# Optimization experiments

Hardware: AMD Instinct MI355X
Metric: run time of the kernel (lower is better)

Reference implementation:

```python
import jax, jax.numpy as jnp
import numpy as np

VOCAB = 32000
EMBED = 512
HIDDEN = 1024
BATCH = 16
SEQ = 256


def setup_inputs() -> dict:
    key = jax.random.key(0)
    ks = jax.random.split(key, 12)
    E, H, V = EMBED, HIDDEN, VOCAB
    s_gate = 1.0 / np.sqrt(E + H)
    s_out = 1.0 / np.sqrt(H)
    return {
        "input": jax.random.randint(ks[0], (BATCH, SEQ), 0, V, dtype=jnp.int32),
        "embed": jax.random.normal(ks[1], (V, E), dtype=jnp.float32),
        "W_f": jax.random.normal(ks[2], (E + H, H), dtype=jnp.float32) * s_gate,
        "b_f": jax.random.normal(ks[3], (H,), dtype=jnp.float32) * s_gate,
        "W_i": jax.random.normal(ks[4], (E + H, H), dtype=jnp.float32) * s_gate,
        "b_i": jax.random.normal(ks[5], (H,), dtype=jnp.float32) * s_gate,
        "W_c": jax.random.normal(ks[6], (E + H, H), dtype=jnp.float32) * s_gate,
        "b_c": jax.random.normal(ks[7], (H,), dtype=jnp.float32) * s_gate,
        "W_o": jax.random.normal(ks[8], (E + H, H), dtype=jnp.float32) * s_gate,
        "b_o": jax.random.normal(ks[9], (H,), dtype=jnp.float32) * s_gate,
        "W_out": jax.random.normal(ks[10], (H, V), dtype=jnp.float32) * s_out,
        "b_out": jax.random.normal(ks[11], (V,), dtype=jnp.float32) * s_out,
    }


def reference(input, embed, W_f, b_f, W_i, b_i, W_c, b_c, W_o, b_o, W_out, b_out):
    B = input.shape[0]
    H = W_f.shape[1]
    tokens = embed[input]                     # [B, S, E]
    xs = jnp.swapaxes(tokens, 0, 1)           # [S, B, E] for scan over time

    def step(carry, x_t):
        h, c = carry
        catted = jnp.concatenate([x_t, h], axis=1)   # [B, E+H]
        f = jax.nn.sigmoid(catted @ W_f + b_f)
        i = jax.nn.sigmoid(catted @ W_i + b_i)
        cand = jnp.tanh(catted @ W_c + b_c)
        o = jax.nn.sigmoid(catted @ W_o + b_o)
        c = c * f + cand * i
        h = c * o
        return (h, c), h

    h0 = jnp.zeros((B, H), dtype=tokens.dtype)
    c0 = jnp.zeros((B, H), dtype=tokens.dtype)
    _, hs = jax.lax.scan(step, (h0, c0), xs)  # hs: [S, B, H]
    hiddens = jnp.swapaxes(hs, 0, 1)          # [B, S, H]
    return hiddens @ W_out + b_out            # [B, S, V]
```

## Files before the change

kernel.cpp:

```cpp
#include <hip/hip_runtime.h>
#include <hip/hip_bf16.h>

#define VOCAB  32000
#define EMBED  512
#define HIDDEN 1024
#define BATCH  16
#define SEQ    256
#define NROW   (BATCH*SEQ)
#define GCOLS  (4*HIDDEN)
#define NWREC  64
#define NWPACK 192
#define NTILE  8000
#define SENT32 0xFFFFFFFFu

typedef unsigned short u16;
typedef unsigned int   u32;
typedef unsigned long long u64;
typedef __attribute__((ext_vector_type(4))) float f32x4;
typedef __attribute__((ext_vector_type(8))) short bf16x8;
typedef __attribute__((ext_vector_type(8))) unsigned short u16x8;
typedef __attribute__((ext_vector_type(2))) unsigned long long u64x2;

__device__ inline u16 f2bf(float f){
  __hip_bfloat16 h = __float2bfloat16(f);
  return __builtin_bit_cast(u16, h);
}
__device__ inline void gload_lds16(const void* g, void* l){
  __builtin_amdgcn_global_load_lds((const __attribute__((address_space(1))) u32*)g,
                                   (__attribute__((address_space(3))) u32*)l, 16, 0, 0);
}
__device__ __forceinline__ u32 al32(const u32* p){
  return __hip_atomic_load(p, __ATOMIC_RELAXED, __HIP_MEMORY_SCOPE_AGENT);
}
__device__ __forceinline__ u64 al64(const u64* p){
  return __hip_atomic_load(p, __ATOMIC_RELAXED, __HIP_MEMORY_SCOPE_AGENT);
}
__device__ __forceinline__ void as32(u32* p, u32 v){
  __hip_atomic_store(p, v, __ATOMIC_RELAXED, __HIP_MEMORY_SCOPE_AGENT);
}
__device__ __forceinline__ void as64(u64* p, u64 v){
  __hip_atomic_store(p, v, __ATOMIC_RELAXED, __HIP_MEMORY_SCOPE_AGENT);
}

__global__ __launch_bounds__(256) void pack_gates(
    const float* __restrict__ Wf, const float* __restrict__ Wi,
    const float* __restrict__ Wc, const float* __restrict__ Wo,
    const float* __restrict__ bf_, const float* __restrict__ bi_,
    const float* __restrict__ bc_, const float* __restrict__ bo_,
    u16* __restrict__ Wxp, u16* __restrict__ Whp, float* __restrict__ bcat)
{
  const int NT_WX = (GCOLS/16)*(EMBED/32)*64;
  const int NT_WH = (GCOLS/16)*(HIDDEN/32)*64;
  int t = blockIdx.x*256 + threadIdx.x;
  if (t < NT_WX){
    int u = t;
    int lane = u&63; int kb = (u>>6)&15; int nblk = u>>10;
    int col = nblk*16 + (lane&15);
    int k0  = kb*32 + ((lane>>4)<<3);
    int g = col>>10, j = col&1023;
    const float* W = (g==0)?Wf:(g==1)?Wi:(g==2)?Wc:Wo;
    u16x8 v;
    #pragma unroll
    for (int e=0;e<8;e++) v[e] = f2bf(W[(size_t)(k0+e)*HIDDEN + j]);
    *(u16x8*)(Wxp + (size_t)u*8) = v;
  } else if (t < NT_WX + NT_WH){
    int u = t - NT_WX;
    int lane = u&63; int kb = (u>>6)&31; int nblk = u>>11;
    int col = nblk*16 + (lane&15);
    int k0  = kb*32 + ((lane>>4)<<3);
    int g = col>>10, j = col&1023;
    const float* W = (g==0)?Wf:(g==1)?Wi:(g==2)?Wc:Wo;
    u16x8 v;
    #pragma unroll
    for (int e=0;e<8;e++) v[e] = f2bf(W[(size_t)(EMBED + k0+e)*HIDDEN + j]);
    *(u16x8*)(Whp + (size_t)u*8) = v;
  } else {
    int u = t - NT_WX - NT_WH;
    if (u < GCOLS){
      int g = u>>10, j = u&1023;
      const float* B = (g==0)?bf_:(g==1)?bi_:(g==2)?bc_:bo_;
      bcat[u] = B[j];
    }
  }
}

__global__ __launch_bounds__(256) void gather_kernel(
    const int* __restrict__ tok, const float* __restrict__ embed, u16* __restrict__ Xg)
{
  int t = blockIdx.x*256 + threadIdx.x;
  int lane = t&63; int kb = (t>>6)&15; int mblk = t>>10;
  int s = mblk; int b = lane&15;
  int token = tok[b*SEQ + s];
  int k0 = kb*32 + ((lane>>4)<<3);
  const float* src = embed + (size_t)token*EMBED + k0;
  u16x8 v;
  #pragma unroll
  for (int e=0;e<8;e++) v[e] = f2bf(src[e]);
  *(u16x8*)(Xg + (size_t)t*8) = v;
}

template<int KB, bool REMAP>
__global__ __launch_bounds__(256,2) void gemm_pk(
    const u16* __restrict__ Ap, const u16* __restrict__ Bp,
    const float* __restrict__ bias, float* __restrict__ C,
    int Nblk128, int N)
{
  __shared__ u16 sm[8192];
  int tid = threadIdx.x; int lane = tid&63; int wv = tid>>6;
  int nwg = gridDim.x;
  int bid = blockIdx.x;
  int swz = (bid&7)*(nwg>>3) + (bid>>3);
  int bm = swz / Nblk128, bn = swz % Nblk128;
  int wr = wv>>1, wc = wv&1;
  f32x4 acc[4][4] = {};
  const u16* Abase = Ap + (size_t)(bm*8)*KB*512;
  const u16* Bbase = Bp + (size_t)(bn*8)*KB*512;
  for (int kb=0; kb<KB; ++kb){
    __syncthreads();
    #pragma unroll
    for (int c2=0;c2<4;c2++){
      int chunk = wv*4 + c2;
      const u16* g;
      if (chunk < 8) g = Abase + ((size_t)chunk*KB + kb)*512 + lane*8;
      else           g = Bbase + ((size_t)(chunk-8)*KB + kb)*512 + lane*8;
      gload_lds16(g, sm + chunk*512);
    }
    __syncthreads();
    bf16x8 a[4], b[4];
    #pragma unroll
    for (int m=0;m<4;m++) a[m] = *(const bf16x8*)(sm + (wr*4+m)*512 + lane*8);
    #pragma unroll
    for (int n=0;n<4;n++) b[n] = *(const bf16x8*)(sm + 4096 + (wc*4+n)*512 + lane*8);
    #pragma unroll
    for (int m=0;m<4;m++)
      #pragma unroll
      for (int n=0;n<4;n++)
        acc[m][n] = __builtin_amdgcn_mfma_f32_16x16x32_bf16(a[m], b[n], acc[m][n], 0,0,0);
  }
  int colb = bn*128 + wc*64;
  int rowb = bm*128 + wr*64;
  #pragma unroll
  for (int m=0;m<4;m++){
    int row0 = rowb + m*16 + (lane>>4)*4;
    #pragma unroll
    for (int n=0;n<4;n++){
      int col = colb + n*16 + (lane&15);
      float bv = bias[col];
      #pragma unroll
      for (int r2=0;r2<4;r2++){
        int row = row0 + r2;
        int orow = REMAP ? ((row&15)*SEQ + (row>>4)) : row;
        C[(size_t)orow*N + col] = acc[m][n][r2] + bv;
      }
    }
  }
}

__global__ __launch_bounds__(256,1) void lstm_fused(
    const u16* __restrict__ Whp, const float* __restrict__ Xpre,
    u16* hb, u16* Hp, u32* cnt, u32* tix, u32* packdone,
    const float* __restrict__ Wout, u16* __restrict__ Woutp,
    const float* __restrict__ bout, float* __restrict__ out)
{
  __shared__ char SMEM[148480];
  __shared__ u32 s_tick;
  u16* smWf = (u16*)SMEM;
  float (*gl)[16][17] = (float (*)[16][17])(SMEM + 131072);
  u16* smg = (u16*)SMEM;

  int tid = threadIdx.x; int lane = tid&63; int v = tid>>6;
  int w = blockIdx.x;

  if (w >= NWREC){
    const int NPK = (VOCAB/16)*(HIDDEN/32)*64;
    int u0 = (w - NWREC)*256 + tid;
    for (int u = u0; u < NPK; u += NWPACK*256){
      int l = u&63; int kb = (u>>6)&31; int nblk = u>>11;
      int col = nblk*16 + (l&15);
      int k0  = kb*32 + ((l>>4)<<3);
      u16x8 vv;
      #pragma unroll
      for (int e=0;e<8;e++) vv[e] = f2bf(Wout[(size_t)(k0+e)*VOCAB + col]);
      u64x2 t2 = __builtin_bit_cast(u64x2, vv);
      u64* dst = (u64*)(Woutp + (size_t)u*8);
      as64(dst+0, t2[0]);
      as64(dst+1, t2[1]);
    }
    asm volatile("s_waitcnt vmcnt(0)" ::: "memory");
    __syncthreads();
    if (tid==0) (void)__hip_atomic_fetch_add(packdone, 1u,
                       __ATOMIC_RELAXED, __HIP_MEMORY_SCOPE_AGENT);
  } else {
    #pragma unroll
    for (int f=0; f<32; ++f){
      int frag = v*32 + f;
      int g = frag>>5, kc = frag&31;
      const u16* src = Whp + ((size_t)(g*64 + w)*32 + kc)*512 + lane*8;
      gload_lds16(src, smWf + (size_t)frag*512);
    }
    asm volatile("s_waitcnt vmcnt(0)" ::: "memory");
    __syncthreads();

    float c = 0.f;
    int pb = tid>>4, pj = tid&15;
    int j = w*16 + pj;
    const int a_row = lane&15, a_k = (lane>>4)*8;
    const float* xb0 = Xpre + (size_t)pb*GCOLS + j;
    float x0 = xb0[0], x1 = xb0[1024], x2 = xb0[2048], x3 = xb0[3072];

    for (int s=0;s<SEQ;s++){
      const u16* rbuf = hb + (size_t)s*16384;
      u64 vv[16];
      for(;;){
        #pragma unroll
        for (int i=0;i<16;i++){
          const u64* p = (const u64*)(rbuf + a_row*1024 + (v*8+(i>>1))*32 + a_k) + (i&1);
          vv[i] = al64(p);
        }
        bool ok = true;
        #pragma unroll
        for (int i=0;i<16;i++)
          ok &= ((u32)vv[i]!=SENT32) & ((u32)(vv[i]>>32)!=SENT32);
        if (ok) break;
        __builtin_amdgcn_s_sleep(1);
      }
      bf16x8 af[8];
      #pragma unroll
      for (int i=0;i<8;i++){
        u64x2 t2 = {vv[2*i], vv[2*i+1]};
        af[i] = __builtin_bit_cast(bf16x8, t2);
      }
      f32x4 acc[4] = {};
      #pragma unroll
      for (int i=0;i<8;i++){
        #pragma unroll
        for (int g=0;g<4;g++){
          bf16x8 wfv = *(const bf16x8*)(smWf + ((size_t)(g*32 + v*8 + i))*512 + lane*8);
          acc[g] = __builtin_amdgcn_mfma_f32_16x16x32_bf16(af[i], wfv, acc[g], 0,0,0);
        }
      }
      {
        int jj = lane&15, b0 = (lane>>4)*4;
        #pragma unroll
        for (int g=0;g<4;g++)
          #pragma unroll
          for (int r2=0;r2<4;r2++)
            gl[v*4+g][b0+r2][jj] = acc[g][r2];
      }
      asm volatile("s_waitcnt lgkmcnt(0)" ::: "memory");
      __builtin_amdgcn_s_barrier();
      __builtin_amdgcn_sched_barrier(0);
      float xn0=0.f,xn1=0.f,xn2=0.f,xn3=0.f;
      if (s < SEQ-1){
        const float* xn = Xpre + ((size_t)(s+1)*16 + pb)*GCOLS + j;
        xn0 = xn[0]; xn1 = xn[1024]; xn2 = xn[2048]; xn3 = xn[3072];
      }
      float p0 = x0 + gl[0][pb][pj] + gl[4][pb][pj] + gl[ 8][pb][pj] + gl[12][pb][pj];
      float p1 = x1 + gl[1][pb][pj] + gl[5][pb][pj] + gl[ 9][pb][pj] + gl[13][pb][pj];
      float p2 = x2 + gl[2][pb][pj] + gl[6][pb][pj] + gl[10][pb][pj] + gl[14][pb][pj];
      float p3 = x3 + gl[3][pb][pj] + gl[7][pb][pj] + gl[11][pb][pj] + gl[15][pb][pj];
      float fg = 1.f/(1.f+__expf(-p0));
      float ig = 1.f/(1.f+__expf(-p1));
      float e2 = __expf(2.f*fminf(fmaxf(p2,-15.f),15.f));
      float cand = (e2-1.f)/(e2+1.f);
      float og = 1.f/(1.f+__expf(-p3));
      c = c*fg + cand*ig;
      float h = c*og;
      x0 = xn0; x1 = xn1; x2 = xn2; x3 = xn3;
      u32 hw_ = (u32)f2bf(h);
      u32 ow_ = (u32)__shfl_xor((int)hw_, 1);
      if ((pj&1)==0){
        u32 word = hw_ | (ow_<<16);
        if (s < SEQ-1){
          u16* wstep = hb + (size_t)(s+1)*16384;
          as32((u32*)wstep + (size_t)pb*512 + w*8 + (pj>>1), word);
        }
        as32((u32*)Hp + (size_t)s*8192 + (size_t)(j>>5)*256
                      + (size_t)(((j>>3)&3)*16 + pb)*4 + ((j&7)>>1), word);
      }
      __builtin_amdgcn_s_barrier();
      __builtin_amdgcn_sched_barrier(0);
      if ((s&7)==7){
        asm volatile("s_waitcnt vmcnt(0)" ::: "memory");
        __builtin_amdgcn_s_barrier();
        asm volatile("" ::: "memory");
        if (tid==0)
          (void)__hip_atomic_fetch_add(cnt + (size_t)(s>>3)*16, 1u,
                   __ATOMIC_RELAXED, __HIP_MEMORY_SCOPE_AGENT);
      }
    }
  }

  if (tid==0){
    while (al32(packdone) < (u32)NWPACK) __builtin_amdgcn_s_sleep(2);
  }
  __syncthreads();

  int wv = tid>>6;
  int wr = wv>>1, wc = wv&1;
  for(;;){
    __syncthreads();
    if (tid==0) s_tick = __hip_atomic_fetch_add(tix, 1u,
                   __ATOMIC_RELAXED, __HIP_MEMORY_SCOPE_AGENT);
    __syncthreads();
    u32 t = s_tick;
    if (t >= (u32)NTILE) break;
    int bm = (int)(t/250u), bn = (int)(t%250u);
    if (tid==0){
      while (al32(cnt + (size_t)bm*16) < (u32)NWREC)
        __builtin_amdgcn_s_sleep(2);
    }
    __syncthreads();
    const u16* Ab = Hp + (size_t)(bm*8)*32*512;
    const u16* Bb = Woutp + (size_t)(bn*8)*32*512;
    auto stage = [&](int kb, int bi){
      #pragma unroll
      for (int c2=0;c2<4;c2++){
        int chunk = wv*4 + c2;
        const u16* g;
        if (chunk < 8) g = Ab + ((size_t)chunk*32 + kb)*512 + lane*8;
        else           g = Bb + ((size_t)(chunk-8)*32 + kb)*512 + lane*8;
        gload_lds16(g, smg + (size_t)bi*8192 + chunk*512);
      }
    };
    stage(0,0); stage(1,1);
    f32x4 acc[4][4] = {};
    for (int kb=0; kb<32; ++kb){
      if (kb<31) asm volatile("s_waitcnt vmcnt(4)" ::: "memory");
      else       asm volatile("s_waitcnt vmcnt(0)" ::: "memory");
      __builtin_amdgcn_s_barrier();
      if (kb+2<32) stage(kb+2, (kb+2)%3);
      const u16* bufp = smg + (size_t)(kb%3)*8192;
      bf16x8 a[4], b[4];
      #pragma unroll
      for (int m=0;m<4;m++) a[m] = *(const bf16x8*)(bufp + (wr*4+m)*512 + lane*8);
      #pragma unroll
      for (int n=0;n<4;n++) b[n] = *(const bf16x8*)(bufp + 4096 + (wc*4+n)*512 + lane*8);
      #pragma unroll
      for (int m=0;m<4;m++)
        #pragma unroll
        for (int n=0;n<4;n++)
          acc[m][n] = __builtin_amdgcn_mfma_f32_16x16x32_bf16(a[m], b[n], acc[m][n], 0,0,0);
    }
    int colb = bn*128 + wc*64;
    int rowb = bm*128 + wr*64;
    #pragma unroll
    for (int m=0;m<4;m++){
      int row0 = rowb + m*16 + (lane>>4)*4;
      #pragma unroll
      for (int n=0;n<4;n++){
        int col = colb + n*16 + (lane&15);
        float bv = bout[col];
        #pragma unroll
        for (int r2=0;r2<4;r2++){
          int row = row0 + r2;
          int orow = (row&15)*SEQ + (row>>4);
          __builtin_nontemporal_store(acc[m][n][r2] + bv,
                                      &out[(size_t)orow*VOCAB + col]);
        }
      }
    }
  }
}

extern "C" void kernel_launch(void* const* d_in, const int* in_sizes, int n_in,
                              void* d_out, int out_size, void* d_ws, size_t ws_size,
                              hipStream_t stream)
{
  (void)in_sizes; (void)n_in; (void)out_size; (void)ws_size;
  const int*   tok   = (const int*)d_in[0];
  const float* embed = (const float*)d_in[1];
  const float* Wf    = (const float*)d_in[2];
  const float* bf_   = (const float*)d_in[3];
  const float* Wi    = (const float*)d_in[4];
  const float* bi_   = (const float*)d_in[5];
  const float* Wc    = (const float*)d_in[6];
  const float* bc_   = (const float*)d_in[7];
  const float* Wo    = (const float*)d_in[8];
  const float* bo_   = (const float*)d_in[9];
  const float* Wout  = (const float*)d_in[10];
  const float* bout  = (const float*)d_in[11];
  float* out = (float*)d_out;

  char* ws = (char*)d_ws;
  size_t off = 0;
  auto alloc = [&](size_t bytes)->void*{
    void* p = ws + off; off += (bytes + 255) & ~(size_t)255; return p;
  };
  u16*  Wxp   = (u16*)alloc((size_t)2097152*2);
  u16*  Xg    = (u16*)alloc((size_t)2097152*2);
  float* bcat = (float*)alloc((size_t)4096*4);
  u16*  hb    = (u16*)ws;
  u16*  Whp   = (u16*)alloc((size_t)4194304*2);
  u16*  Woutp = (u16*)alloc((size_t)32768000*2);
  float* Xpre = (float*)alloc((size_t)NROW*GCOLS*4);
  u16*  Hp    = (u16*)alloc((size_t)4194304*2);
  u32*  cnt   = (u32*)alloc((size_t)4096);
  u32*  tix   = (u32*)alloc((size_t)256);
  u32*  packdone = (u32*)alloc((size_t)256);

  pack_gates<<<3088, 256, 0, stream>>>(Wf,Wi,Wc,Wo, bf_,bi_,bc_,bo_,
                                       Wxp, Whp, bcat);
  gather_kernel<<<1024, 256, 0, stream>>>(tok, embed, Xg);
  gemm_pk<16,false><<<1024, 256, 0, stream>>>(Xg, Wxp, bcat, Xpre, 32, GCOLS);
  (void)hipMemsetAsync(hb, 0x00, 32768, stream);
  (void)hipMemsetAsync((char*)hb + 32768, 0xFF, 255*32768, stream);
  (void)hipMemsetAsync(cnt, 0, 4096 + 256 + 256, stream);
  lstm_fused<<<NWREC+NWPACK, 256, 0, stream>>>(Whp, Xpre, hb, Hp, cnt, tix,
                                               packdone, Wout, Woutp, bout, out);
}
```

Before: 1.169 ms.

## Replace per-step hidden buffer with double-buffered per-workgroup mailboxes

Instead of one shared hidden-state buffer per timestep that all 64 recurrent workgroups poll, each workgroup now gets its own double-buffered mailbox copy. Each writer broadcasts its h words into all 32 consumer copies, and readers reset their slot to the sentinel after consuming it. The aim is to cut contention on shared cache lines during the spin-wait and shrink the memset footprint. The next-step Xpre loads are also hoisted earlier, poll sleep intervals are raised, and output tiles are reordered so four row-blocks share a column tile. In exchange this adds many more global stores per step and a vmcnt wait before the broadcast.

```diff
diff --git a/kernel.cpp b/kernel.cpp
--- a/kernel.cpp
+++ b/kernel.cpp
@@ -158,7 +158,7 @@
 
 __global__ __launch_bounds__(256,1) void lstm_fused(
     const u16* __restrict__ Whp, const float* __restrict__ Xpre,
-    u16* hb, u16* Hp, u32* cnt, u32* tix, u32* packdone,
+    u16* mbox, u16* Hp, u32* cnt, u32* tix, u32* packdone,
     const float* __restrict__ Wout, u16* __restrict__ Woutp,
     const float* __restrict__ bout, float* __restrict__ out)
 {
@@ -209,12 +209,12 @@
     float x0 = xb0[0], x1 = xb0[1024], x2 = xb0[2048], x3 = xb0[3072];
 
     for (int s=0;s<SEQ;s++){
-      const u16* rbuf = hb + (size_t)s*16384;
+      const u16* rb = mbox + (size_t)((s+1)&1)*1048576 + (size_t)w*16384;
       u64 vv[16];
       for(;;){
         #pragma unroll
         for (int i=0;i<16;i++){
-          const u64* p = (const u64*)(rbuf + a_row*1024 + (v*8+(i>>1))*32 + a_k) + (i&1);
+          const u64* p = (const u64*)(rb + a_row*1024 + (v*8+(i>>1))*32 + a_k) + (i&1);
           vv[i] = al64(p);
         }
         bool ok = true;
@@ -224,6 +224,18 @@
         if (ok) break;
         __builtin_amdgcn_s_sleep(1);
       }
+      if (s < SEQ-1){
+        #pragma unroll
+        for (int i=0;i<16;i++){
+          u64* p = (u64*)(rb + a_row*1024 + (v*8+(i>>1))*32 + a_k) + (i&1);
+          as64(p, ~0ull);
+        }
+      }
+      float xn0=0.f,xn1=0.f,xn2=0.f,xn3=0.f;
+      if (s < SEQ-1){
+        const float* xn = Xpre + ((size_t)(s+1)*16 + pb)*GCOLS + j;
+        xn0 = xn[0]; xn1 = xn[1024]; xn2 = xn[2048]; xn3 = xn[3072];
+      }
       bf16x8 af[8];
       #pragma unroll
       for (int i=0;i<8;i++){
@@ -250,11 +262,6 @@
       asm volatile("s_waitcnt lgkmcnt(0)" ::: "memory");
       __builtin_amdgcn_s_barrier();
       __builtin_amdgcn_sched_barrier(0);
-      float xn0=0.f,xn1=0.f,xn2=0.f,xn3=0.f;
-      if (s < SEQ-1){
-        const float* xn = Xpre + ((size_t)(s+1)*16 + pb)*GCOLS + j;
-        xn0 = xn[0]; xn1 = xn[1024]; xn2 = xn[2048]; xn3 = xn[3072];
-      }
       float p0 = x0 + gl[0][pb][pj] + gl[4][pb][pj] + gl[ 8][pb][pj] + gl[12][pb][pj];
       float p1 = x1 + gl[1][pb][pj] + gl[5][pb][pj] + gl[ 9][pb][pj] + gl[13][pb][pj];
       float p2 = x2 + gl[2][pb][pj] + gl[6][pb][pj] + gl[10][pb][pj] + gl[14][pb][pj];
@@ -267,14 +274,21 @@
       c = c*fg + cand*ig;
       float h = c*og;
       x0 = xn0; x1 = xn1; x2 = xn2; x3 = xn3;
-      u32 hw_ = (u32)f2bf(h);
-      u32 ow_ = (u32)__shfl_xor((int)hw_, 1);
+      asm volatile("s_waitcnt vmcnt(0)" ::: "memory");
+      u32 hb16 = (u32)f2bf(h);
+      u32 nb   = (u32)__shfl_xor((int)hb16, 1);
+      u32 word = (pj&1) ? ((hb16<<16) | nb) : (hb16 | (nb<<16));
+      if (s < SEQ-1){
+        u32* mb = (u32*)mbox + (size_t)(s&1)*524288
+                + (size_t)pb*512 + w*8 + (pj>>1);
+        int c0 = (pj&1) ? 32 : 0;
+        #pragma unroll
+        for (int cc=0; cc<32; cc++){
+          int cdst = c0 + ((w + cc) & 31);
+          as32(mb + (size_t)cdst*8192, word);
+        }
+      }
       if ((pj&1)==0){
-        u32 word = hw_ | (ow_<<16);
-        if (s < SEQ-1){
-          u16* wstep = hb + (size_t)(s+1)*16384;
-          as32((u32*)wstep + (size_t)pb*512 + w*8 + (pj>>1), word);
-        }
         as32((u32*)Hp + (size_t)s*8192 + (size_t)(j>>5)*256
                       + (size_t)(((j>>3)&3)*16 + pb)*4 + ((j&7)>>1), word);
       }
@@ -292,7 +306,7 @@
   }
 
   if (tid==0){
-    while (al32(packdone) < (u32)NWPACK) __builtin_amdgcn_s_sleep(2);
+    while (al32(packdone) < (u32)NWPACK) __builtin_amdgcn_s_sleep(8);
   }
   __syncthreads();
 
@@ -305,10 +319,12 @@
     __syncthreads();
     u32 t = s_tick;
     if (t >= (u32)NTILE) break;
-    int bm = (int)(t/250u), bn = (int)(t%250u);
+    u32 rr = t / 1000u, local = t % 1000u;
+    int bn = (int)(local >> 2);
+    int bm = (int)(rr*4u + (local & 3u));
     if (tid==0){
       while (al32(cnt + (size_t)bm*16) < (u32)NWREC)
-        __builtin_amdgcn_s_sleep(2);
+        __builtin_amdgcn_s_sleep(8);
     }
     __syncthreads();
     const u16* Ab = Hp + (size_t)(bm*8)*32*512;
@@ -390,7 +406,7 @@
   u16*  Wxp   = (u16*)alloc((size_t)2097152*2);
   u16*  Xg    = (u16*)alloc((size_t)2097152*2);
   float* bcat = (float*)alloc((size_t)4096*4);
-  u16*  hb    = (u16*)ws;
+  u16*  mbox  = (u16*)ws;
   u16*  Whp   = (u16*)alloc((size_t)4194304*2);
   u16*  Woutp = (u16*)alloc((size_t)32768000*2);
   float* Xpre = (float*)alloc((size_t)NROW*GCOLS*4);
@@ -403,9 +419,9 @@
                                        Wxp, Whp, bcat);
   gather_kernel<<<1024, 256, 0, stream>>>(tok, embed, Xg);
   gemm_pk<16,false><<<1024, 256, 0, stream>>>(Xg, Wxp, bcat, Xpre, 32, GCOLS);
-  (void)hipMemsetAsync(hb, 0x00, 32768, stream);
-  (void)hipMemsetAsync((char*)hb + 32768, 0xFF, 255*32768, stream);
+  (void)hipMemsetAsync(mbox, 0xFF, 2097152, stream);
+  (void)hipMemsetAsync((char*)mbox + 2097152, 0x00, 2097152, stream);
   (void)hipMemsetAsync(cnt, 0, 4096 + 256 + 256, stream);
-  lstm_fused<<<NWREC+NWPACK, 256, 0, stream>>>(Whp, Xpre, hb, Hp, cnt, tix,
+  lstm_fused<<<NWREC+NWPACK, 256, 0, stream>>>(Whp, Xpre, mbox, Hp, cnt, tix,
                                                packdone, Wout, Woutp, bout, out);
 }
```

New measurement: 2.187 ms. 87.0% more time.

## Add per-block canary flags for recurrence sync and deepen output GEMM pipeline

Applied to the files above, without the earlier changes.

The recurrent blocks now poll a small per-step canary word, written by each producer block after its barrier, before reading the full hidden-state buffer. This replaces polling all 16 hidden-state words for sentinels and should cut the memory traffic of spinning. The next-step Xpre loads are issued earlier, the output GEMM goes from a 3-stage to an 8-stage LDS pipeline, and tiles are ordered so four row-blocks share each column-block for better L2 reuse of Woutp. Sleep intervals on the pack and row-ready waits grow. The cost is extra flag stores, a second memset, and more LDS per block.

```diff
diff --git a/kernel.cpp b/kernel.cpp
--- a/kernel.cpp
+++ b/kernel.cpp
@@ -158,7 +158,7 @@
 
 __global__ __launch_bounds__(256,1) void lstm_fused(
     const u16* __restrict__ Whp, const float* __restrict__ Xpre,
-    u16* hb, u16* Hp, u32* cnt, u32* tix, u32* packdone,
+    u16* hb, u16* Hp, u32* cnt, u32* tix, u32* packdone, u32* canary,
     const float* __restrict__ Wout, u16* __restrict__ Woutp,
     const float* __restrict__ bout, float* __restrict__ out)
 {
@@ -210,19 +210,41 @@
 
     for (int s=0;s<SEQ;s++){
       const u16* rbuf = hb + (size_t)s*16384;
+      const u32* cyp = canary + ((size_t)s*64 + (size_t)v*16 + (lane&15))*32;
       u64 vv[16];
-      for(;;){
+      {
         #pragma unroll
         for (int i=0;i<16;i++){
           const u64* p = (const u64*)(rbuf + a_row*1024 + (v*8+(i>>1))*32 + a_k) + (i&1);
           vv[i] = al64(p);
         }
-        bool ok = true;
-        #pragma unroll
-        for (int i=0;i<16;i++)
-          ok &= ((u32)vv[i]!=SENT32) & ((u32)(vv[i]>>32)!=SENT32);
-        if (ok) break;
-        __builtin_amdgcn_s_sleep(1);
+        u32 cv = al32(cyp);
+        if (!__all(cv != 0u)){
+          do { __builtin_amdgcn_s_sleep(1); cv = al32(cyp); } while (!__all(cv != 0u));
+          #pragma unroll
+          for (int i=0;i<16;i++){
+            const u64* p = (const u64*)(rbuf + a_row*1024 + (v*8+(i>>1))*32 + a_k) + (i&1);
+            vv[i] = al64(p);
+          }
+        }
+        for(;;){
+          bool ok = true;
+          #pragma unroll
+          for (int i=0;i<16;i++)
+            ok &= ((u32)vv[i]!=SENT32) & ((u32)(vv[i]>>32)!=SENT32);
+          if (ok) break;
+          __builtin_amdgcn_s_sleep(0);
+          #pragma unroll
+          for (int i=0;i<16;i++){
+            const u64* p = (const u64*)(rbuf + a_row*1024 + (v*8+(i>>1))*32 + a_k) + (i&1);
+            vv[i] = al64(p);
+          }
+        }
+      }
+      float xn0=0.f,xn1=0.f,xn2=0.f,xn3=0.f;
+      if (s < SEQ-1){
+        const float* xn = Xpre + ((size_t)(s+1)*16 + pb)*GCOLS + j;
+        xn0 = xn[0]; xn1 = xn[1024]; xn2 = xn[2048]; xn3 = xn[3072];
       }
       bf16x8 af[8];
       #pragma unroll
@@ -250,11 +272,6 @@
       asm volatile("s_waitcnt lgkmcnt(0)" ::: "memory");
       __builtin_amdgcn_s_barrier();
       __builtin_amdgcn_sched_barrier(0);
-      float xn0=0.f,xn1=0.f,xn2=0.f,xn3=0.f;
-      if (s < SEQ-1){
-        const float* xn = Xpre + ((size_t)(s+1)*16 + pb)*GCOLS + j;
-        xn0 = xn[0]; xn1 = xn[1024]; xn2 = xn[2048]; xn3 = xn[3072];
-      }
       float p0 = x0 + gl[0][pb][pj] + gl[4][pb][pj] + gl[ 8][pb][pj] + gl[12][pb][pj];
       float p1 = x1 + gl[1][pb][pj] + gl[5][pb][pj] + gl[ 9][pb][pj] + gl[13][pb][pj];
       float p2 = x2 + gl[2][pb][pj] + gl[6][pb][pj] + gl[10][pb][pj] + gl[14][pb][pj];
@@ -280,6 +297,8 @@
       }
       __builtin_amdgcn_s_barrier();
       __builtin_amdgcn_sched_barrier(0);
+      if (tid==0 && s < SEQ-1)
+        as32(canary + ((size_t)(s+1)*64 + w)*32, 1u);
       if ((s&7)==7){
         asm volatile("s_waitcnt vmcnt(0)" ::: "memory");
         __builtin_amdgcn_s_barrier();
@@ -292,7 +311,7 @@
   }
 
   if (tid==0){
-    while (al32(packdone) < (u32)NWPACK) __builtin_amdgcn_s_sleep(2);
+    while (al32(packdone) < (u32)NWPACK) __builtin_amdgcn_s_sleep(8);
   }
   __syncthreads();
 
@@ -305,10 +324,12 @@
     __syncthreads();
     u32 t = s_tick;
     if (t >= (u32)NTILE) break;
-    int bm = (int)(t/250u), bn = (int)(t%250u);
+    u32 rr = t / 1000u, local = t % 1000u;
+    int bn = (int)(local >> 2);
+    int bm = (int)(rr*4u + (local & 3u));
     if (tid==0){
       while (al32(cnt + (size_t)bm*16) < (u32)NWREC)
-        __builtin_amdgcn_s_sleep(2);
+        __builtin_amdgcn_s_sleep(8);
     }
     __syncthreads();
     const u16* Ab = Hp + (size_t)(bm*8)*32*512;
@@ -323,14 +344,20 @@
         gload_lds16(g, smg + (size_t)bi*8192 + chunk*512);
       }
     };
-    stage(0,0); stage(1,1);
+    #pragma unroll
+    for (int k=0;k<7;k++) stage(k, k);
     f32x4 acc[4][4] = {};
     for (int kb=0; kb<32; ++kb){
-      if (kb<31) asm volatile("s_waitcnt vmcnt(4)" ::: "memory");
-      else       asm volatile("s_waitcnt vmcnt(0)" ::: "memory");
+      if      (kb <= 25) asm volatile("s_waitcnt vmcnt(24)" ::: "memory");
+      else if (kb == 26) asm volatile("s_waitcnt vmcnt(20)" ::: "memory");
+      else if (kb == 27) asm volatile("s_waitcnt vmcnt(16)" ::: "memory");
+      else if (kb == 28) asm volatile("s_waitcnt vmcnt(12)" ::: "memory");
+      else if (kb == 29) asm volatile("s_waitcnt vmcnt(8)"  ::: "memory");
+      else if (kb == 30) asm volatile("s_waitcnt vmcnt(4)"  ::: "memory");
+      else               asm volatile("s_waitcnt vmcnt(0)"  ::: "memory");
       __builtin_amdgcn_s_barrier();
-      if (kb+2<32) stage(kb+2, (kb+2)%3);
-      const u16* bufp = smg + (size_t)(kb%3)*8192;
+      if (kb <= 24) stage(kb+7, (kb+7)&7);
+      const u16* bufp = smg + (size_t)(kb&7)*8192;
       bf16x8 a[4], b[4];
       #pragma unroll
       for (int m=0;m<4;m++) a[m] = *(const bf16x8*)(bufp + (wr*4+m)*512 + lane*8);
@@ -398,6 +425,7 @@
   u32*  cnt   = (u32*)alloc((size_t)4096);
   u32*  tix   = (u32*)alloc((size_t)256);
   u32*  packdone = (u32*)alloc((size_t)256);
+  u32*  canary = (u32*)alloc((size_t)SEQ*64*128);
 
   pack_gates<<<3088, 256, 0, stream>>>(Wf,Wi,Wc,Wo, bf_,bi_,bc_,bo_,
                                        Wxp, Whp, bcat);
@@ -406,6 +434,8 @@
   (void)hipMemsetAsync(hb, 0x00, 32768, stream);
   (void)hipMemsetAsync((char*)hb + 32768, 0xFF, 255*32768, stream);
   (void)hipMemsetAsync(cnt, 0, 4096 + 256 + 256, stream);
+  (void)hipMemsetAsync(canary, 0x01, 64*128, stream);
+  (void)hipMemsetAsync((char*)canary + 64*128, 0x00, (SEQ-1)*64*128, stream);
   lstm_fused<<<NWREC+NWPACK, 256, 0, stream>>>(Whp, Xpre, hb, Hp, cnt, tix,
-                                               packdone, Wout, Woutp, bout, out);
-}
+                                               packdone, canary, Wout, Woutp, bout, out);
+}
```

Result: slower. 1.452 ms (+24.1%).

## Replace sentinel polling on hidden state with per-step per-block arrival flags

Applied to the files above, without the earlier changes.

The recurrent blocks no longer spin on the hidden-state buffer checking for a 0xFF sentinel. Each block now writes its h slice, waits for its stores to drain, and sets a per-step flag; consumers poll 64 flags (one per lane of wave 0) with atomic RMWs before loading h once. This drops the 8 MB sentinel memset and the repeated wide polling loads, but adds a vmcnt drain and a full barrier on every step. The output GEMM tile order is also remapped to group 4 row blocks per N sweep, and the sleep intervals for packing and tile waits are lengthened.

```diff
diff --git a/kernel.cpp b/kernel.cpp
--- a/kernel.cpp
+++ b/kernel.cpp
@@ -11,7 +11,6 @@
 #define NWREC  64
 #define NWPACK 192
 #define NTILE  8000
-#define SENT32 0xFFFFFFFFu
 
 typedef unsigned short u16;
 typedef unsigned int   u32;
@@ -40,6 +39,9 @@
 }
 __device__ __forceinline__ void as64(u64* p, u64 v){
   __hip_atomic_store(p, v, __ATOMIC_RELAXED, __HIP_MEMORY_SCOPE_AGENT);
+}
+__device__ __forceinline__ u32 armw(u32* p, u32 v){
+  return __hip_atomic_fetch_add(p, v, __ATOMIC_RELAXED, __HIP_MEMORY_SCOPE_AGENT);
 }
 
 __global__ __launch_bounds__(256) void pack_gates(
@@ -158,7 +160,7 @@
 
 __global__ __launch_bounds__(256,1) void lstm_fused(
     const u16* __restrict__ Whp, const float* __restrict__ Xpre,
-    u16* hb, u16* Hp, u32* cnt, u32* tix, u32* packdone,
+    u16* hb, u16* Hp, u32* cnt, u32* tix, u32* packdone, u32* flags,
     const float* __restrict__ Wout, u16* __restrict__ Woutp,
     const float* __restrict__ bout, float* __restrict__ out)
 {
@@ -188,8 +190,7 @@
     }
     asm volatile("s_waitcnt vmcnt(0)" ::: "memory");
     __syncthreads();
-    if (tid==0) (void)__hip_atomic_fetch_add(packdone, 1u,
-                       __ATOMIC_RELAXED, __HIP_MEMORY_SCOPE_AGENT);
+    if (tid==0) (void)armw(packdone, 1u);
   } else {
     #pragma unroll
     for (int f=0; f<32; ++f){
@@ -209,20 +210,24 @@
     float x0 = xb0[0], x1 = xb0[1024], x2 = xb0[2048], x3 = xb0[3072];
 
     for (int s=0;s<SEQ;s++){
+      if (s > 0){
+        if (v==0){
+          u32* fl = flags + ((size_t)s*64 + lane)*32;
+          for(;;){
+            u32 old = armw(fl, 0u);
+            if (__all(old != 0u)) break;
+            __builtin_amdgcn_s_sleep(1);
+          }
+        }
+        __builtin_amdgcn_s_barrier();
+        asm volatile("" ::: "memory");
+      }
       const u16* rbuf = hb + (size_t)s*16384;
       u64 vv[16];
-      for(;;){
-        #pragma unroll
-        for (int i=0;i<16;i++){
-          const u64* p = (const u64*)(rbuf + a_row*1024 + (v*8+(i>>1))*32 + a_k) + (i&1);
-          vv[i] = al64(p);
-        }
-        bool ok = true;
-        #pragma unroll
-        for (int i=0;i<16;i++)
-          ok &= ((u32)vv[i]!=SENT32) & ((u32)(vv[i]>>32)!=SENT32);
-        if (ok) break;
-        __builtin_amdgcn_s_sleep(1);
+      #pragma unroll
+      for (int i=0;i<16;i++){
+        const u64* p = (const u64*)(rbuf + a_row*1024 + (v*8+(i>>1))*32 + a_k) + (i&1);
+        vv[i] = al64(p);
       }
       bf16x8 af[8];
       #pragma unroll
@@ -278,21 +283,20 @@
         as32((u32*)Hp + (size_t)s*8192 + (size_t)(j>>5)*256
                       + (size_t)(((j>>3)&3)*16 + pb)*4 + ((j&7)>>1), word);
       }
+      asm volatile("s_waitcnt vmcnt(0)" ::: "memory");
       __builtin_amdgcn_s_barrier();
-      __builtin_amdgcn_sched_barrier(0);
-      if ((s&7)==7){
-        asm volatile("s_waitcnt vmcnt(0)" ::: "memory");
-        __builtin_amdgcn_s_barrier();
-        asm volatile("" ::: "memory");
-        if (tid==0)
-          (void)__hip_atomic_fetch_add(cnt + (size_t)(s>>3)*16, 1u,
-                   __ATOMIC_RELAXED, __HIP_MEMORY_SCOPE_AGENT);
+      asm volatile("" ::: "memory");
+      if (tid==0){
+        if (s < SEQ-1)
+          (void)armw(flags + ((size_t)(s+1)*64 + w)*32, 1u);
+        if ((s&7)==7)
+          (void)armw(cnt + (size_t)(s>>3)*16, 1u);
       }
     }
   }
 
   if (tid==0){
-    while (al32(packdone) < (u32)NWPACK) __builtin_amdgcn_s_sleep(2);
+    while (al32(packdone) < (u32)NWPACK) __builtin_amdgcn_s_sleep(8);
   }
   __syncthreads();
 
@@ -300,15 +304,16 @@
   int wr = wv>>1, wc = wv&1;
   for(;;){
     __syncthreads();
-    if (tid==0) s_tick = __hip_atomic_fetch_add(tix, 1u,
-                   __ATOMIC_RELAXED, __HIP_MEMORY_SCOPE_AGENT);
+    if (tid==0) s_tick = armw(tix, 1u);
     __syncthreads();
     u32 t = s_tick;
     if (t >= (u32)NTILE) break;
-    int bm = (int)(t/250u), bn = (int)(t%250u);
+    u32 rr = t / 1000u, local = t % 1000u;
+    int bn = (int)(local >> 2);
+    int bm = (int)(rr*4u + (local & 3u));
     if (tid==0){
       while (al32(cnt + (size_t)bm*16) < (u32)NWREC)
-        __builtin_amdgcn_s_sleep(2);
+        __builtin_amdgcn_s_sleep(8);
     }
     __syncthreads();
     const u16* Ab = Hp + (size_t)(bm*8)*32*512;
@@ -398,14 +403,15 @@
   u32*  cnt   = (u32*)alloc((size_t)4096);
   u32*  tix   = (u32*)alloc((size_t)256);
   u32*  packdone = (u32*)alloc((size_t)256);
+  u32*  flags = (u32*)alloc((size_t)SEQ*64*128);
 
   pack_gates<<<3088, 256, 0, stream>>>(Wf,Wi,Wc,Wo, bf_,bi_,bc_,bo_,
                                        Wxp, Whp, bcat);
   gather_kernel<<<1024, 256, 0, stream>>>(tok, embed, Xg);
   gemm_pk<16,false><<<1024, 256, 0, stream>>>(Xg, Wxp, bcat, Xpre, 32, GCOLS);
   (void)hipMemsetAsync(hb, 0x00, 32768, stream);
-  (void)hipMemsetAsync((char*)hb + 32768, 0xFF, 255*32768, stream);
   (void)hipMemsetAsync(cnt, 0, 4096 + 256 + 256, stream);
+  (void)hipMemsetAsync(flags, 0, (size_t)SEQ*64*128, stream);
   lstm_fused<<<NWREC+NWPACK, 256, 0, stream>>>(Whp, Xpre, hb, Hp, cnt, tix,
-                                               packdone, Wout, Woutp, bout, out);
-}
+                                               packdone, flags, Wout, Woutp, bout, out);
+}
```

Result: slower. 1.258 ms (+7.5%).
